# Optimization experiments

Measured on AMD Instinct MI355X. Metric: run time of the kernel, lower is better.

The kernel has to match this reference:

```python
import jax, jax.numpy as jnp
import numpy as np

B, L, H, E, D = 4, 2048, 8, 64, 64  # seq S == L (causal mask requires square scores)


def setup_inputs() -> dict:
    key = jax.random.key(0)
    k0, k1, k2, k3, k4 = jax.random.split(key, 5)
    queries = jax.random.normal(k0, (B, L, H, E), jnp.float32)
    keys = jax.random.normal(k1, (B, L, H, E), jnp.float32)
    values = jax.random.normal(k2, (B, L, H, D), jnp.float32)
    # per-sample learned de-stationary scale (positive) and bias
    tau = jax.random.uniform(k3, (B, 1, 1), jnp.float32, 0.5, 1.5)
    delta = jax.random.normal(k4, (B, 1, L), jnp.float32) * 0.1
    return {"queries": queries, "keys": keys, "values": values, "tau": tau, "delta": delta}


def reference(queries, keys, values, tau, delta):
    Bq, Lq, Hq, Eq = queries.shape
    S = keys.shape[1]
    scale = 1.0 / jnp.sqrt(jnp.asarray(Eq, jnp.float32))
    # torch path: rearrange('b s h d l -> (b d) s h l') with s=h=d=1 -> [B,1,1,1] / [B,1,1,S]
    tau_b = tau.reshape(Bq, 1, 1, 1)
    delta_b = delta.reshape(Bq, 1, 1, -1)[..., :S]
    # scores: [B, H, L, S]
    scores = jnp.einsum('blhe,bshe->bhls', queries, keys) * tau_b + delta_b
    causal = jnp.triu(jnp.ones((Lq, S), bool), k=1)  # True above diagonal -> masked
    scores = jnp.where(causal, -jnp.inf, scores)
    A = jax.nn.softmax(scale * scores, axis=-1)  # dropout is identity in eval/reference
    V = jnp.einsum('bhls,bshd->blhd', A, values)  # [B, L, H, D]
    return V
```

## Files before the change

kernel.cpp:

```cpp
#include <hip/hip_runtime.h>
#include <hip/hip_bf16.h>

#define Bsz 4
#define Lsz 2048
#define Hsz 8

typedef __attribute__((ext_vector_type(8))) short bf16x8;
typedef __attribute__((ext_vector_type(4))) short bf16x4;
typedef __attribute__((ext_vector_type(4))) float f32x4;

__device__ __forceinline__ short f2bs(float f) {
    union { float f; unsigned u; } v; v.f = f;
    unsigned r = v.u + 0x7FFFu + ((v.u >> 16) & 1u);
    return (short)(r >> 16);
}
__device__ __forceinline__ short f2bs_rh(float f) {
    return (short)((__float_as_uint(f) + 0x8000u) >> 16);
}

__device__ __forceinline__ void stage16(const short* g, short* l) {
    __builtin_amdgcn_global_load_lds(
        (const __attribute__((address_space(1))) unsigned int*)g,
        (__attribute__((address_space(3))) unsigned int*)l,
        16, 0, 0);
}

__global__ __launch_bounds__(256) void prep_kv(
    const float* __restrict__ ksrc, const float* __restrict__ vsrc,
    short* __restrict__ Kf, short* __restrict__ Vf)
{
    __shared__ float Tl[64][65];
    const int raw = blockIdx.x;
    const int tid = threadIdx.x;
    const bool isK = raw < Bsz*Hsz*32;
    const int bid = isK ? raw : raw - Bsz*Hsz*32;
    const int tl = bid & 31, bh = bid >> 5;
    const int b = bh >> 3, h = bh & 7;

    const int row = tid >> 2, c0 = (tid & 3) * 16;
    const float* src = (isK ? ksrc : vsrc)
                     + (((size_t)b*Lsz + tl*64 + row)*Hsz + h)*64 + c0;
    *(float4*)&Tl[row][c0]      = *(const float4*)(src);
    *(float4*)&Tl[row][c0 + 4]  = *(const float4*)(src + 4);
    *(float4*)&Tl[row][c0 + 8]  = *(const float4*)(src + 8);
    *(float4*)&Tl[row][c0 + 12] = *(const float4*)(src + 12);
    __syncthreads();

    const int lane = tid & 63, ln = lane & 15, quad = lane >> 4;
    if (isK) {
        short* dst = Kf + (size_t)bid * 4096;
        #pragma unroll
        for (int cc = 0; cc < 2; ++cc) {
            const int c  = (tid >> 6)*2 + cc;
            const int nt = c >> 1, eh = c & 1;
            const float* rp = &Tl[nt*16 + ln][eh*32 + quad*8];
            bf16x8 o = {f2bs(rp[0]),f2bs(rp[1]),f2bs(rp[2]),f2bs(rp[3]),
                        f2bs(rp[4]),f2bs(rp[5]),f2bs(rp[6]),f2bs(rp[7])};
            *(bf16x8*)(dst + c*512 + lane*8) = o;
        }
    } else {
        short* dst = Vf + (size_t)bid * 4096;
        #pragma unroll
        for (int cc = 0; cc < 2; ++cc) {
            const int cp  = (tid >> 6)*2 + cc;
            const int m16 = cp >> 1, nt0 = (cp & 1)*2;
            const int d   = m16*16 + ln;
            const int s0  = nt0*16 + quad*4;
            bf16x8 o = {f2bs(Tl[s0+0][d]),  f2bs(Tl[s0+1][d]),
                        f2bs(Tl[s0+2][d]),  f2bs(Tl[s0+3][d]),
                        f2bs(Tl[s0+16][d]), f2bs(Tl[s0+17][d]),
                        f2bs(Tl[s0+18][d]), f2bs(Tl[s0+19][d])};
            *(bf16x8*)(dst + cp*512 + lane*8) = o;
        }
    }
}

__global__ __launch_bounds__(256, 4) void dsattn_main(
    const float* __restrict__ q,
    const short* __restrict__ Kf,
    const short* __restrict__ Vf,
    const float* __restrict__ tau,
    const float* __restrict__ delta,
    float* __restrict__ out)
{
    __shared__ __align__(16) short Kb[2][4096];
    __shared__ __align__(16) short Vb[2][4096];
    __shared__ float dls[Lsz];

    const int tid  = threadIdx.x;
    const int wv   = tid >> 6;
    const int lane = tid & 63;
    const int ln   = lane & 15;
    const int quad = lane >> 4;

    const int bh = blockIdx.x;
    const int b  = bh >> 3, h = bh & 7;
    const int j  = blockIdx.y, aj = j & 7, gj = j >> 3;
    const int qt = (gj == 0) ? aj : (gj == 1) ? 15 - aj
                 : (gj == 2) ? 16 + aj : 31 - aj;
    const int q0 = qt * 64;
    const int T  = qt + 1;

    const float c2  = 0.125f * 1.44269504f;
    const float st2 = c2 * tau[b];

    const short* kt = Kf + (size_t)bh * (32*4096);
    const short* vt = Vf + (size_t)bh * (32*4096);

    {
        const float* dsrc = delta + (size_t)b*Lsz + tid*8;
        float4 a = *(const float4*)(dsrc);
        float4 c = *(const float4*)(dsrc + 4);
        a.x*=c2; a.y*=c2; a.z*=c2; a.w*=c2;
        c.x*=c2; c.y*=c2; c.z*=c2; c.w*=c2;
        *(float4*)&dls[tid*8]     = a;
        *(float4*)&dls[tid*8 + 4] = c;
    }

    #pragma unroll
    for (int u = 0; u < 4; ++u) {
        const int c = wv*4 + u;
        const short* g = ((c < 8) ? kt : vt) + (c & 7)*512 + lane*8;
        short* l = ((c < 8) ? &Kb[0][0] : &Vb[0][0]) + (c & 7)*512;
        stage16(g, l);
    }

    bf16x8 qf0, qf1;
    {
        const float* qrow = q + (((size_t)b*Lsz + q0 + wv*16 + ln)*Hsz + h)*64;
        float4 a0 = *(const float4*)(qrow + quad*8);
        float4 a1 = *(const float4*)(qrow + quad*8 + 4);
        float4 b0 = *(const float4*)(qrow + 32 + quad*8);
        float4 b1 = *(const float4*)(qrow + 32 + quad*8 + 4);
        qf0 = (bf16x8){f2bs(a0.x),f2bs(a0.y),f2bs(a0.z),f2bs(a0.w),
                       f2bs(a1.x),f2bs(a1.y),f2bs(a1.z),f2bs(a1.w)};
        qf1 = (bf16x8){f2bs(b0.x),f2bs(b0.y),f2bs(b0.z),f2bs(b0.w),
                       f2bs(b1.x),f2bs(b1.y),f2bs(b1.z),f2bs(b1.w)};
    }

    f32x4 oacc[4];
    #pragma unroll
    for (int m = 0; m < 4; ++m) oacc[m] = (f32x4){0.f,0.f,0.f,0.f};
    float l_acc = 0.f;

    __syncthreads();

    for (int t = 0; t < T; ++t) {
        const int cur = t & 1;
        if (t + 1 < T) {
            const int nb = cur ^ 1;
            #pragma unroll
            for (int u = 0; u < 4; ++u) {
                const int c = wv*4 + u;
                const short* g = ((c < 8) ? kt : vt)
                               + (size_t)(t+1)*4096 + (c & 7)*512 + lane*8;
                short* l = ((c < 8) ? &Kb[nb][0] : &Vb[nb][0]) + (c & 7)*512;
                stage16(g, l);
            }
        }

        const short* Kc = &Kb[cur][0];
        const short* Vc = &Vb[cur][0];
        const int k0 = t*64;

        f32x4 sacc[4];
        #pragma unroll
        for (int nt = 0; nt < 4; ++nt) {
            bf16x8 kf0 = *(const bf16x8*)(Kc + (nt*2+0)*512 + lane*8);
            bf16x8 kf1 = *(const bf16x8*)(Kc + (nt*2+1)*512 + lane*8);
            f32x4 z = (f32x4){0.f,0.f,0.f,0.f};
            z = __builtin_amdgcn_mfma_f32_16x16x32_bf16(kf0, qf0, z, 0,0,0);
            sacc[nt] = __builtin_amdgcn_mfma_f32_16x16x32_bf16(kf1, qf1, z, 0,0,0);
        }

        f32x4 dlv[4];
        #pragma unroll
        for (int nt = 0; nt < 4; ++nt)
            dlv[nt] = *(const f32x4*)&dls[k0 + nt*16 + quad*4];

        if (t == qt) {
            const int qrow = q0 + wv*16 + ln;
            #pragma unroll
            for (int nt = 0; nt < 4; ++nt)
                #pragma unroll
                for (int r = 0; r < 4; ++r)
                    if (k0 + nt*16 + quad*4 + r > qrow) sacc[nt][r] = -1e30f;
        }
        bf16x4 pT[4];
        #pragma unroll
        for (int nt = 0; nt < 4; ++nt) {
            float p0 = __builtin_amdgcn_exp2f(fmaf(sacc[nt][0], st2, dlv[nt][0]));
            float p1 = __builtin_amdgcn_exp2f(fmaf(sacc[nt][1], st2, dlv[nt][1]));
            float p2 = __builtin_amdgcn_exp2f(fmaf(sacc[nt][2], st2, dlv[nt][2]));
            float p3 = __builtin_amdgcn_exp2f(fmaf(sacc[nt][3], st2, dlv[nt][3]));
            l_acc += (p0 + p1) + (p2 + p3);
            pT[nt] = (bf16x4){f2bs_rh(p0), f2bs_rh(p1), f2bs_rh(p2), f2bs_rh(p3)};
        }

        #pragma unroll
        for (int ntp = 0; ntp < 2; ++ntp)
            #pragma unroll
            for (int m16 = 0; m16 < 4; ++m16) {
                bf16x8 vv = *(const bf16x8*)(Vc + (m16*2+ntp)*512 + lane*8);
                bf16x4 v0 = (bf16x4){vv[0], vv[1], vv[2], vv[3]};
                bf16x4 v1 = (bf16x4){vv[4], vv[5], vv[6], vv[7]};
                oacc[m16] = __builtin_amdgcn_mfma_f32_16x16x16bf16_1k(
                    v0, pT[2*ntp+0], oacc[m16], 0,0,0);
                oacc[m16] = __builtin_amdgcn_mfma_f32_16x16x16bf16_1k(
                    v1, pT[2*ntp+1], oacc[m16], 0,0,0);
            }

        __syncthreads();
    }

    float lsum = l_acc;
    lsum += __shfl_xor(lsum, 16, 64);
    lsum += __shfl_xor(lsum, 32, 64);
    const float inv = 1.0f / lsum;
    const int qrow = q0 + wv*16 + ln;
    float* orow = out + (((size_t)b*Lsz + qrow)*Hsz + h)*64;
    #pragma unroll
    for (int m16 = 0; m16 < 4; ++m16) {
        float4 o = {oacc[m16][0]*inv, oacc[m16][1]*inv,
                    oacc[m16][2]*inv, oacc[m16][3]*inv};
        *(float4*)(orow + m16*16 + quad*4) = o;
    }
}

extern "C" void kernel_launch(void* const* d_in, const int* in_sizes, int n_in,
                              void* d_out, int out_size, void* d_ws, size_t ws_size,
                              hipStream_t stream) {
    (void)in_sizes; (void)n_in; (void)out_size; (void)ws_size;
    const float* q     = (const float*)d_in[0];
    const float* k     = (const float*)d_in[1];
    const float* v     = (const float*)d_in[2];
    const float* tau   = (const float*)d_in[3];
    const float* delta = (const float*)d_in[4];
    float* out = (float*)d_out;

    short* Kf = (short*)d_ws;
    short* Vf = (short*)d_ws + (size_t)(4*1024*1024);

    prep_kv<<<dim3(Bsz*Hsz*32*2), dim3(256), 0, stream>>>(k, v, Kf, Vf);
    dsattn_main<<<dim3(Bsz*Hsz, 32), dim3(256), 0, stream>>>(q, Kf, Vf, tau, delta, out);
}
```

Before: 126.9 us.

## Software-pipeline QK of next tile with softmax and PV of previous tile

Restructures the attention loop so that the QK MFMA for tile t runs alongside the exp/softmax and PV MFMA for tile t-1. Score registers alternate between two sets, and V fragments are preloaded into registers before each barrier. Staging is also reorganised so each wave issues four contiguous 16-byte global-to-LDS loads per tile, with pointer increments instead of recomputed addresses, and s_setprio is raised around the compute section. This aims to hide exp latency and LDS read latency behind matrix work, at the cost of higher register pressure and more complex prologue and epilogue code for the causal diagonal tile.

```diff
diff --git a/kernel.cpp b/kernel.cpp
--- a/kernel.cpp
+++ b/kernel.cpp
@@ -107,6 +107,19 @@
     const short* kt = Kf + (size_t)bh * (32*4096);
     const short* vt = Vf + (size_t)bh * (32*4096);
 
+    const short* gsrc = ((wv < 2) ? kt : vt) + (wv & 1)*2048 + lane*8;
+
+#define STAGE(buf) do {                                                     \
+        short* lb_ = (wv < 2 ? &Kb[(buf)][0] : &Vb[(buf)][0]) + (wv&1)*2048;\
+        stage16(gsrc + 0*512, lb_ + 0*512);                                 \
+        stage16(gsrc + 1*512, lb_ + 1*512);                                 \
+        stage16(gsrc + 2*512, lb_ + 2*512);                                 \
+        stage16(gsrc + 3*512, lb_ + 3*512);                                 \
+        gsrc += 4096;                                                       \
+    } while (0)
+
+    STAGE(0);
+
     {
         const float* dsrc = delta + (size_t)b*Lsz + tid*8;
         float4 a = *(const float4*)(dsrc);
@@ -115,14 +128,6 @@
         c.x*=c2; c.y*=c2; c.z*=c2; c.w*=c2;
         *(float4*)&dls[tid*8]     = a;
         *(float4*)&dls[tid*8 + 4] = c;
-    }
-
-    #pragma unroll
-    for (int u = 0; u < 4; ++u) {
-        const int c = wv*4 + u;
-        const short* g = ((c < 8) ? kt : vt) + (c & 7)*512 + lane*8;
-        short* l = ((c < 8) ? &Kb[0][0] : &Vb[0][0]) + (c & 7)*512;
-        stage16(g, l);
     }
 
     bf16x8 qf0, qf1;
@@ -141,76 +146,102 @@
     f32x4 oacc[4];
     #pragma unroll
     for (int m = 0; m < 4; ++m) oacc[m] = (f32x4){0.f,0.f,0.f,0.f};
+    f32x4 sE[4], sO[4];
+    bf16x8 vv[8];
+    bf16x4 pT[4];
     float l_acc = 0.f;
 
+#define QK(tt, SW) do {                                                     \
+        const short* Kc_ = &Kb[(tt)&1][0];                                  \
+        _Pragma("unroll")                                                   \
+        for (int nt = 0; nt < 4; ++nt) {                                    \
+            bf16x8 kf0_ = *(const bf16x8*)(Kc_ + (nt*2+0)*512 + lane*8);    \
+            bf16x8 kf1_ = *(const bf16x8*)(Kc_ + (nt*2+1)*512 + lane*8);    \
+            f32x4 z_ = (f32x4){0.f,0.f,0.f,0.f};                            \
+            z_ = __builtin_amdgcn_mfma_f32_16x16x32_bf16(kf0_, qf0, z_, 0,0,0); \
+            (SW)[nt] = __builtin_amdgcn_mfma_f32_16x16x32_bf16(kf1_, qf1, z_, 0,0,0); \
+        }                                                                   \
+    } while (0)
+
+#define SM(tm, SR) do {                                                     \
+        const int k0_ = (tm)*64;                                            \
+        _Pragma("unroll")                                                   \
+        for (int nt = 0; nt < 4; ++nt) {                                    \
+            f32x4 dlv_ = *(const f32x4*)&dls[k0_ + nt*16 + quad*4];         \
+            float p0_ = __builtin_amdgcn_exp2f(fmaf((SR)[nt][0], st2, dlv_[0])); \
+            float p1_ = __builtin_amdgcn_exp2f(fmaf((SR)[nt][1], st2, dlv_[1])); \
+            float p2_ = __builtin_amdgcn_exp2f(fmaf((SR)[nt][2], st2, dlv_[2])); \
+            float p3_ = __builtin_amdgcn_exp2f(fmaf((SR)[nt][3], st2, dlv_[3])); \
+            l_acc += (p0_ + p1_) + (p2_ + p3_);                             \
+            pT[nt] = (bf16x4){f2bs_rh(p0_), f2bs_rh(p1_),                   \
+                              f2bs_rh(p2_), f2bs_rh(p3_)};                  \
+        }                                                                   \
+    } while (0)
+
+#define PV() do {                                                           \
+        _Pragma("unroll")                                                   \
+        for (int ntp = 0; ntp < 2; ++ntp)                                   \
+            _Pragma("unroll")                                               \
+            for (int m16 = 0; m16 < 4; ++m16) {                             \
+                bf16x8 v8_ = vv[m16*2 + ntp];                               \
+                bf16x4 v0_ = (bf16x4){v8_[0], v8_[1], v8_[2], v8_[3]};      \
+                bf16x4 v1_ = (bf16x4){v8_[4], v8_[5], v8_[6], v8_[7]};      \
+                oacc[m16] = __builtin_amdgcn_mfma_f32_16x16x16bf16_1k(      \
+                    v0_, pT[2*ntp+0], oacc[m16], 0,0,0);                    \
+                oacc[m16] = __builtin_amdgcn_mfma_f32_16x16x16bf16_1k(      \
+                    v1_, pT[2*ntp+1], oacc[m16], 0,0,0);                    \
+            }                                                               \
+    } while (0)
+
+#define VLOAD(tt) do {                                                      \
+        const short* Vc_ = &Vb[(tt)&1][0];                                  \
+        _Pragma("unroll")                                                   \
+        for (int c = 0; c < 8; ++c)                                         \
+            vv[c] = *(const bf16x8*)(Vc_ + c*512 + lane*8);                 \
+    } while (0)
+
+#define BODY(tt, SW, SR) do {                                               \
+        if ((tt) + 1 < T) STAGE(((tt)+1)&1);                                \
+        __builtin_amdgcn_s_setprio(1);                                      \
+        QK((tt), SW);                  \
+        SM((tt)-1, SR);                \
+        PV();                          \
+        __builtin_amdgcn_s_setprio(0);                                      \
+        VLOAD(tt);                     \
+        __syncthreads();                                                    \
+    } while (0)
+
     __syncthreads();
 
-    for (int t = 0; t < T; ++t) {
-        const int cur = t & 1;
-        if (t + 1 < T) {
-            const int nb = cur ^ 1;
+    if (T > 1) STAGE(1);
+    __builtin_amdgcn_s_setprio(1);
+    QK(0, sE);
+    __builtin_amdgcn_s_setprio(0);
+    VLOAD(0);
+    __syncthreads();
+
+    int t = 1;
+    for (; t + 1 < T; t += 2) {
+        BODY(t,     sO, sE);
+        BODY(t + 1, sE, sO);
+    }
+    if (t < T) BODY(t, sO, sE);
+
+    if ((T - 1) & 1) {
+        #pragma unroll
+        for (int nt = 0; nt < 4; ++nt) sE[nt] = sO[nt];
+    }
+
+    {
+        const int k0 = (T - 1) * 64;
+        const int qrow = q0 + wv*16 + ln;
+        #pragma unroll
+        for (int nt = 0; nt < 4; ++nt)
             #pragma unroll
-            for (int u = 0; u < 4; ++u) {
-                const int c = wv*4 + u;
-                const short* g = ((c < 8) ? kt : vt)
-                               + (size_t)(t+1)*4096 + (c & 7)*512 + lane*8;
-                short* l = ((c < 8) ? &Kb[nb][0] : &Vb[nb][0]) + (c & 7)*512;
-                stage16(g, l);
-            }
-        }
-
-        const short* Kc = &Kb[cur][0];
-        const short* Vc = &Vb[cur][0];
-        const int k0 = t*64;
-
-        f32x4 sacc[4];
-        #pragma unroll
-        for (int nt = 0; nt < 4; ++nt) {
-            bf16x8 kf0 = *(const bf16x8*)(Kc + (nt*2+0)*512 + lane*8);
-            bf16x8 kf1 = *(const bf16x8*)(Kc + (nt*2+1)*512 + lane*8);
-            f32x4 z = (f32x4){0.f,0.f,0.f,0.f};
-            z = __builtin_amdgcn_mfma_f32_16x16x32_bf16(kf0, qf0, z, 0,0,0);
-            sacc[nt] = __builtin_amdgcn_mfma_f32_16x16x32_bf16(kf1, qf1, z, 0,0,0);
-        }
-
-        f32x4 dlv[4];
-        #pragma unroll
-        for (int nt = 0; nt < 4; ++nt)
-            dlv[nt] = *(const f32x4*)&dls[k0 + nt*16 + quad*4];
-
-        if (t == qt) {
-            const int qrow = q0 + wv*16 + ln;
-            #pragma unroll
-            for (int nt = 0; nt < 4; ++nt)
-                #pragma unroll
-                for (int r = 0; r < 4; ++r)
-                    if (k0 + nt*16 + quad*4 + r > qrow) sacc[nt][r] = -1e30f;
-        }
-        bf16x4 pT[4];
-        #pragma unroll
-        for (int nt = 0; nt < 4; ++nt) {
-            float p0 = __builtin_amdgcn_exp2f(fmaf(sacc[nt][0], st2, dlv[nt][0]));
-            float p1 = __builtin_amdgcn_exp2f(fmaf(sacc[nt][1], st2, dlv[nt][1]));
-            float p2 = __builtin_amdgcn_exp2f(fmaf(sacc[nt][2], st2, dlv[nt][2]));
-            float p3 = __builtin_amdgcn_exp2f(fmaf(sacc[nt][3], st2, dlv[nt][3]));
-            l_acc += (p0 + p1) + (p2 + p3);
-            pT[nt] = (bf16x4){f2bs_rh(p0), f2bs_rh(p1), f2bs_rh(p2), f2bs_rh(p3)};
-        }
-
-        #pragma unroll
-        for (int ntp = 0; ntp < 2; ++ntp)
-            #pragma unroll
-            for (int m16 = 0; m16 < 4; ++m16) {
-                bf16x8 vv = *(const bf16x8*)(Vc + (m16*2+ntp)*512 + lane*8);
-                bf16x4 v0 = (bf16x4){vv[0], vv[1], vv[2], vv[3]};
-                bf16x4 v1 = (bf16x4){vv[4], vv[5], vv[6], vv[7]};
-                oacc[m16] = __builtin_amdgcn_mfma_f32_16x16x16bf16_1k(
-                    v0, pT[2*ntp+0], oacc[m16], 0,0,0);
-                oacc[m16] = __builtin_amdgcn_mfma_f32_16x16x16bf16_1k(
-                    v1, pT[2*ntp+1], oacc[m16], 0,0,0);
-            }
-
-        __syncthreads();
+            for (int r = 0; r < 4; ++r)
+                if (k0 + nt*16 + quad*4 + r > qrow) sE[nt][r] = -1e30f;
+        SM(T - 1, sE);
+        PV();
     }
 
     float lsum = l_acc;
@@ -225,6 +256,12 @@
                     oacc[m16][2]*inv, oacc[m16][3]*inv};
         *(float4*)(orow + m16*16 + quad*4) = o;
     }
+#undef STAGE
+#undef QK
+#undef SM
+#undef PV
+#undef VLOAD
+#undef BODY
 }
 
 extern "C" void kernel_launch(void* const* d_in, const int* in_sizes, int n_in,
```

New measurement: 125.6 us. About the same (-1.0%).

## Split key tiles across waves with shared Q and cross-wave output reduction

Applied to the files above, without the earlier changes.

The main kernel now gives each wave a 16-key slice of every 64-key tile, and all four waves compute against the full 64-row query block, which is stored once in LDS. This replaces the old scheme where each wave owned 16 query rows. Partial outputs and row sums are combined through LDS at the end, and the scaled delta is precomputed by extra blocks in the prep kernel. Each wave stages only its own K/V chunks, using explicit vmcnt waits instead of a per-tile block barrier, and MFMA sections run at raised priority. The costs are 64 accumulator registers per lane and an LDS reduction epilogue, and the query-tile order is rearranged for load balance.

```diff
diff --git a/kernel.cpp b/kernel.cpp
--- a/kernel.cpp
+++ b/kernel.cpp
@@ -5,9 +5,9 @@
 #define Lsz 2048
 #define Hsz 8
 
-typedef __attribute__((ext_vector_type(8))) short bf16x8;
-typedef __attribute__((ext_vector_type(4))) short bf16x4;
-typedef __attribute__((ext_vector_type(4))) float f32x4;
+typedef __attribute__((ext_vector_type(8)))  short bf16x8;
+typedef __attribute__((ext_vector_type(4)))  short bf16x4;
+typedef __attribute__((ext_vector_type(4)))  float f32x4;
 
 __device__ __forceinline__ short f2bs(float f) {
     union { float f; unsigned u; } v; v.f = f;
@@ -27,11 +27,23 @@
 
 __global__ __launch_bounds__(256) void prep_kv(
     const float* __restrict__ ksrc, const float* __restrict__ vsrc,
-    short* __restrict__ Kf, short* __restrict__ Vf)
+    const float* __restrict__ delta,
+    short* __restrict__ Kf, short* __restrict__ Vf, float* __restrict__ Df)
 {
-    __shared__ float Tl[64][65];
     const int raw = blockIdx.x;
     const int tid = threadIdx.x;
+    if (raw >= 2*Bsz*Hsz*32) {
+        const float c2 = 0.125f * 1.44269504f;
+        const int base = ((raw - 2*Bsz*Hsz*32)*256 + tid) * 16;
+        #pragma unroll
+        for (int u = 0; u < 4; ++u) {
+            float4 v = *(const float4*)(delta + base + u*4);
+            v.x*=c2; v.y*=c2; v.z*=c2; v.w*=c2;
+            *(float4*)(Df + base + u*4) = v;
+        }
+        return;
+    }
+    __shared__ float Tl[64][65];
     const bool isK = raw < Bsz*Hsz*32;
     const int bid = isK ? raw : raw - Bsz*Hsz*32;
     const int tl = bid & 31, bh = bid >> 5;
@@ -52,8 +64,8 @@
         #pragma unroll
         for (int cc = 0; cc < 2; ++cc) {
             const int c  = (tid >> 6)*2 + cc;
-            const int nt = c >> 1, eh = c & 1;
-            const float* rp = &Tl[nt*16 + ln][eh*32 + quad*8];
+            const int kq = c >> 1, eb = c & 1;
+            const float* rp = &Tl[kq*16 + ln][eb*32 + quad*8];
             bf16x8 o = {f2bs(rp[0]),f2bs(rp[1]),f2bs(rp[2]),f2bs(rp[3]),
                         f2bs(rp[4]),f2bs(rp[5]),f2bs(rp[6]),f2bs(rp[7])};
             *(bf16x8*)(dst + c*512 + lane*8) = o;
@@ -62,15 +74,16 @@
         short* dst = Vf + (size_t)bid * 4096;
         #pragma unroll
         for (int cc = 0; cc < 2; ++cc) {
-            const int cp  = (tid >> 6)*2 + cc;
-            const int m16 = cp >> 1, nt0 = (cp & 1)*2;
-            const int d   = m16*16 + ln;
-            const int s0  = nt0*16 + quad*4;
-            bf16x8 o = {f2bs(Tl[s0+0][d]),  f2bs(Tl[s0+1][d]),
-                        f2bs(Tl[s0+2][d]),  f2bs(Tl[s0+3][d]),
-                        f2bs(Tl[s0+16][d]), f2bs(Tl[s0+17][d]),
-                        f2bs(Tl[s0+18][d]), f2bs(Tl[s0+19][d])};
-            *(bf16x8*)(dst + cp*512 + lane*8) = o;
+            const int c   = (tid >> 6)*2 + cc;
+            const int kq  = c >> 1, dgp = c & 1;
+            const int s0  = kq*16 + quad*4;
+            const int d0  = dgp*32 + ln;
+            const int d1  = dgp*32 + 16 + ln;
+            bf16x8 o = {f2bs(Tl[s0+0][d0]), f2bs(Tl[s0+1][d0]),
+                        f2bs(Tl[s0+2][d0]), f2bs(Tl[s0+3][d0]),
+                        f2bs(Tl[s0+0][d1]), f2bs(Tl[s0+1][d1]),
+                        f2bs(Tl[s0+2][d1]), f2bs(Tl[s0+3][d1])};
+            *(bf16x8*)(dst + c*512 + lane*8) = o;
         }
     }
 }
@@ -79,152 +92,206 @@
     const float* __restrict__ q,
     const short* __restrict__ Kf,
     const short* __restrict__ Vf,
+    const float* __restrict__ Df,
     const float* __restrict__ tau,
-    const float* __restrict__ delta,
     float* __restrict__ out)
 {
     __shared__ __align__(16) short Kb[2][4096];
     __shared__ __align__(16) short Vb[2][4096];
-    __shared__ float dls[Lsz];
+    __shared__ __align__(16) short Qs[4096];
 
     const int tid  = threadIdx.x;
-    const int wv   = tid >> 6;
+    const int kq   = tid >> 6;
     const int lane = tid & 63;
     const int ln   = lane & 15;
     const int quad = lane >> 4;
 
     const int bh = blockIdx.x;
     const int b  = bh >> 3, h = bh & 7;
-    const int j  = blockIdx.y, aj = j & 7, gj = j >> 3;
-    const int qt = (gj == 0) ? aj : (gj == 1) ? 15 - aj
-                 : (gj == 2) ? 16 + aj : 31 - aj;
+    const int y = blockIdx.y, g8 = y >> 3, a = y & 7;
+    const int qt = (g8 == 0) ? 31 - 2*a : (g8 == 1) ? 2*a
+                 : (g8 == 2) ? 30 - 2*a : 2*a + 1;
     const int q0 = qt * 64;
     const int T  = qt + 1;
 
-    const float c2  = 0.125f * 1.44269504f;
-    const float st2 = c2 * tau[b];
-
-    const short* kt = Kf + (size_t)bh * (32*4096);
-    const short* vt = Vf + (size_t)bh * (32*4096);
+    const float st2 = (0.125f * 1.44269504f) * tau[b];
+
+    const short* gK = Kf + (size_t)bh*(32*4096) + kq*1024 + lane*8;
+    const short* gV = Vf + (size_t)bh*(32*4096) + kq*1024 + lane*8;
+    const float* Dfp = Df + (size_t)b*Lsz + kq*16 + quad*4;
+
+    short* const myK0 = &Kb[0][kq*1024];
+    short* const myV0 = &Vb[0][kq*1024];
+
+#define STAGE(buf) do {                                                     \
+        short* k_ = (buf) ? myK0 + 4096 : myK0;                             \
+        short* v_ = (buf) ? myV0 + 4096 : myV0;                             \
+        stage16(gK + 0*512, k_ + 0*512);                                    \
+        stage16(gK + 1*512, k_ + 1*512);                                    \
+        stage16(gV + 0*512, v_ + 0*512);                                    \
+        stage16(gV + 1*512, v_ + 1*512);                                    \
+        gK += 4096; gV += 4096;                                             \
+        __builtin_amdgcn_sched_barrier(0);                                  \
+    } while (0)
+#define WAITN(n) do {                                                       \
+        asm volatile("s_waitcnt vmcnt(" #n ")" ::: "memory");               \
+        __builtin_amdgcn_sched_barrier(0);                                  \
+    } while (0)
+
+    STAGE(0);
+    f32x4 dlv_c = *(const f32x4*)(Dfp); Dfp += 64;
 
     {
-        const float* dsrc = delta + (size_t)b*Lsz + tid*8;
-        float4 a = *(const float4*)(dsrc);
-        float4 c = *(const float4*)(dsrc + 4);
-        a.x*=c2; a.y*=c2; a.z*=c2; a.w*=c2;
-        c.x*=c2; c.y*=c2; c.z*=c2; c.w*=c2;
-        *(float4*)&dls[tid*8]     = a;
-        *(float4*)&dls[tid*8 + 4] = c;
-    }
-
-    #pragma unroll
-    for (int u = 0; u < 4; ++u) {
-        const int c = wv*4 + u;
-        const short* g = ((c < 8) ? kt : vt) + (c & 7)*512 + lane*8;
-        short* l = ((c < 8) ? &Kb[0][0] : &Vb[0][0]) + (c & 7)*512;
-        stage16(g, l);
-    }
-
-    bf16x8 qf0, qf1;
-    {
-        const float* qrow = q + (((size_t)b*Lsz + q0 + wv*16 + ln)*Hsz + h)*64;
+        const float* qrow = q + (((size_t)b*Lsz + q0 + kq*16 + ln)*Hsz + h)*64;
         float4 a0 = *(const float4*)(qrow + quad*8);
         float4 a1 = *(const float4*)(qrow + quad*8 + 4);
         float4 b0 = *(const float4*)(qrow + 32 + quad*8);
         float4 b1 = *(const float4*)(qrow + 32 + quad*8 + 4);
-        qf0 = (bf16x8){f2bs(a0.x),f2bs(a0.y),f2bs(a0.z),f2bs(a0.w),
-                       f2bs(a1.x),f2bs(a1.y),f2bs(a1.z),f2bs(a1.w)};
-        qf1 = (bf16x8){f2bs(b0.x),f2bs(b0.y),f2bs(b0.z),f2bs(b0.w),
-                       f2bs(b1.x),f2bs(b1.y),f2bs(b1.z),f2bs(b1.w)};
-    }
-
-    f32x4 oacc[4];
+        bf16x8 q0f = {f2bs(a0.x),f2bs(a0.y),f2bs(a0.z),f2bs(a0.w),
+                      f2bs(a1.x),f2bs(a1.y),f2bs(a1.z),f2bs(a1.w)};
+        bf16x8 q1f = {f2bs(b0.x),f2bs(b0.y),f2bs(b0.z),f2bs(b0.w),
+                      f2bs(b1.x),f2bs(b1.y),f2bs(b1.z),f2bs(b1.w)};
+        *(bf16x8*)(&Qs[(kq*2+0)*512 + lane*8]) = q0f;
+        *(bf16x8*)(&Qs[(kq*2+1)*512 + lane*8]) = q1f;
+    }
+
+    f32x4 oacc[4][4];
     #pragma unroll
-    for (int m = 0; m < 4; ++m) oacc[m] = (f32x4){0.f,0.f,0.f,0.f};
-    float l_acc = 0.f;
-
-    __syncthreads();
-
-    for (int t = 0; t < T; ++t) {
-        const int cur = t & 1;
-        if (t + 1 < T) {
-            const int nb = cur ^ 1;
+    for (int dg = 0; dg < 4; ++dg)
+        #pragma unroll
+        for (int qg = 0; qg < 4; ++qg)
+            oacc[dg][qg] = (f32x4){0.f,0.f,0.f,0.f};
+    float l_acc[4] = {0.f,0.f,0.f,0.f};
+
+    __syncthreads();
+
+#define TILE_BODY(t_, MASKED, HASNEXT) do {                                 \
+        const short* Kc_ = ((t_) & 1) ? myK0 + 4096 : myK0;                 \
+        const short* Vc_ = ((t_) & 1) ? myV0 + 4096 : myV0;                 \
+        f32x4 dlv_n_;                                                       \
+        if (HASNEXT) {                                                      \
+            STAGE(((t_)+1) & 1);                                            \
+            dlv_n_ = *(const f32x4*)(Dfp); Dfp += 64;                       \
+        }                                                                   \
+        if (HASNEXT) WAITN(8); else WAITN(3);            \
+        bf16x8 kf0_ = *(const bf16x8*)(Kc_ + 0*512 + lane*8);               \
+        bf16x8 kf1_ = *(const bf16x8*)(Kc_ + 1*512 + lane*8);               \
+        f32x4 sacc_[4];                                                     \
+        __builtin_amdgcn_s_setprio(1);                                      \
+        _Pragma("unroll")                                                   \
+        for (int qg = 0; qg < 4; ++qg) {                                    \
+            bf16x8 qa_ = *(const bf16x8*)(&Qs[(qg*2+0)*512 + lane*8]);      \
+            bf16x8 qb_ = *(const bf16x8*)(&Qs[(qg*2+1)*512 + lane*8]);      \
+            f32x4 z_ = (f32x4){0.f,0.f,0.f,0.f};                            \
+            z_ = __builtin_amdgcn_mfma_f32_16x16x32_bf16(kf0_, qa_, z_, 0,0,0); \
+            sacc_[qg] = __builtin_amdgcn_mfma_f32_16x16x32_bf16(kf1_, qb_, z_, 0,0,0); \
+        }                                                                   \
+        __builtin_amdgcn_s_setprio(0);                                      \
+        if (MASKED) {                                                       \
+            _Pragma("unroll")                                               \
+            for (int qg = 0; qg < 4; ++qg)                                  \
+                _Pragma("unroll")                                           \
+                for (int r = 0; r < 4; ++r)                                 \
+                    if (kq*16 + quad*4 + r > qg*16 + ln) sacc_[qg][r] = -1e30f; \
+        }                                                                   \
+        bf16x4 pT_[4];                                                      \
+        _Pragma("unroll")                                                   \
+        for (int qg = 0; qg < 4; ++qg) {                                    \
+            float p0_ = __builtin_amdgcn_exp2f(fmaf(sacc_[qg][0], st2, dlv_c[0])); \
+            float p1_ = __builtin_amdgcn_exp2f(fmaf(sacc_[qg][1], st2, dlv_c[1])); \
+            float p2_ = __builtin_amdgcn_exp2f(fmaf(sacc_[qg][2], st2, dlv_c[2])); \
+            float p3_ = __builtin_amdgcn_exp2f(fmaf(sacc_[qg][3], st2, dlv_c[3])); \
+            l_acc[qg] += (p0_ + p1_) + (p2_ + p3_);                         \
+            pT_[qg] = (bf16x4){f2bs_rh(p0_), f2bs_rh(p1_),                  \
+                               f2bs_rh(p2_), f2bs_rh(p3_)};                 \
+        }                                                                   \
+        if (HASNEXT) dlv_c = dlv_n_;                                        \
+        if (HASNEXT) WAITN(5); else WAITN(0);         \
+        bf16x4 vf_[4];                                                      \
+        _Pragma("unroll")                                                   \
+        for (int dg = 0; dg < 4; ++dg)                                      \
+            vf_[dg] = *(const bf16x4*)(Vc_ + (dg>>1)*512 + lane*8 + (dg&1)*4); \
+        __builtin_amdgcn_s_setprio(1);                                      \
+        _Pragma("unroll")                                                   \
+        for (int dg = 0; dg < 4; ++dg)                                      \
+            _Pragma("unroll")                                               \
+            for (int qg = 0; qg < 4; ++qg)                                  \
+                oacc[dg][qg] = __builtin_amdgcn_mfma_f32_16x16x16bf16_1k(   \
+                    vf_[dg], pT_[qg], oacc[dg][qg], 0,0,0);                 \
+        __builtin_amdgcn_s_setprio(0);                                      \
+    } while (0)
+
+    for (int t = 0; t < T - 1; ++t) TILE_BODY(t, false, true);
+    TILE_BODY(T - 1, true, false);
+
+    float lq[4];
+    #pragma unroll
+    for (int qg = 0; qg < 4; ++qg) {
+        float s = l_acc[qg];
+        s += __shfl_xor(s, 16, 64);
+        s += __shfl_xor(s, 32, 64);
+        lq[qg] = s;
+    }
+    float* KbF = (float*)&Kb[0][0];
+    float* VbF = (float*)&Vb[0][0];
+    float* lred = (float*)&Qs[0];
+    __syncthreads();
+
+    if (lane < 16)
+        #pragma unroll
+        for (int qg = 0; qg < 4; ++qg) lred[kq*64 + qg*16 + ln] = lq[qg];
+    if (kq == 1 || kq == 3) {
+        float* dst = (kq == 1) ? KbF : VbF;
+        #pragma unroll
+        for (int dg = 0; dg < 4; ++dg)
             #pragma unroll
-            for (int u = 0; u < 4; ++u) {
-                const int c = wv*4 + u;
-                const short* g = ((c < 8) ? kt : vt)
-                               + (size_t)(t+1)*4096 + (c & 7)*512 + lane*8;
-                short* l = ((c < 8) ? &Kb[nb][0] : &Vb[nb][0]) + (c & 7)*512;
-                stage16(g, l);
+            for (int qg = 0; qg < 4; ++qg)
+                *(f32x4*)(dst + (dg*4+qg)*256 + lane*4) = oacc[dg][qg];
+    }
+    __syncthreads();
+    if (kq == 0 || kq == 2) {
+        const float* srcp = (kq == 0) ? KbF : VbF;
+        #pragma unroll
+        for (int dg = 0; dg < 4; ++dg)
+            #pragma unroll
+            for (int qg = 0; qg < 4; ++qg) {
+                f32x4 v = *(const f32x4*)(srcp + (dg*4+qg)*256 + lane*4);
+                oacc[dg][qg][0] += v[0]; oacc[dg][qg][1] += v[1];
+                oacc[dg][qg][2] += v[2]; oacc[dg][qg][3] += v[3];
+            }
+    }
+    __syncthreads();
+    if (kq == 2) {
+        #pragma unroll
+        for (int dg = 0; dg < 4; ++dg)
+            #pragma unroll
+            for (int qg = 0; qg < 4; ++qg)
+                *(f32x4*)(KbF + (dg*4+qg)*256 + lane*4) = oacc[dg][qg];
+    }
+    __syncthreads();
+    if (kq == 0) {
+        float inv[4];
+        #pragma unroll
+        for (int qg = 0; qg < 4; ++qg)
+            inv[qg] = 1.0f / (lred[qg*16 + ln] + lred[64 + qg*16 + ln]
+                            + lred[128 + qg*16 + ln] + lred[192 + qg*16 + ln]);
+        #pragma unroll
+        for (int qg = 0; qg < 4; ++qg) {
+            float* orow = out + (((size_t)b*Lsz + q0 + qg*16 + ln)*Hsz + h)*64;
+            #pragma unroll
+            for (int dg = 0; dg < 4; ++dg) {
+                f32x4 v = *(const f32x4*)(KbF + (dg*4+qg)*256 + lane*4);
+                float4 o = {(oacc[dg][qg][0] + v[0]) * inv[qg],
+                            (oacc[dg][qg][1] + v[1]) * inv[qg],
+                            (oacc[dg][qg][2] + v[2]) * inv[qg],
+                            (oacc[dg][qg][3] + v[3]) * inv[qg]};
+                *(float4*)(orow + dg*16 + quad*4) = o;
             }
         }
-
-        const short* Kc = &Kb[cur][0];
-        const short* Vc = &Vb[cur][0];
-        const int k0 = t*64;
-
-        f32x4 sacc[4];
-        #pragma unroll
-        for (int nt = 0; nt < 4; ++nt) {
-            bf16x8 kf0 = *(const bf16x8*)(Kc + (nt*2+0)*512 + lane*8);
-            bf16x8 kf1 = *(const bf16x8*)(Kc + (nt*2+1)*512 + lane*8);
-            f32x4 z = (f32x4){0.f,0.f,0.f,0.f};
-            z = __builtin_amdgcn_mfma_f32_16x16x32_bf16(kf0, qf0, z, 0,0,0);
-            sacc[nt] = __builtin_amdgcn_mfma_f32_16x16x32_bf16(kf1, qf1, z, 0,0,0);
-        }
-
-        f32x4 dlv[4];
-        #pragma unroll
-        for (int nt = 0; nt < 4; ++nt)
-            dlv[nt] = *(const f32x4*)&dls[k0 + nt*16 + quad*4];
-
-        if (t == qt) {
-            const int qrow = q0 + wv*16 + ln;
-            #pragma unroll
-            for (int nt = 0; nt < 4; ++nt)
-                #pragma unroll
-                for (int r = 0; r < 4; ++r)
-                    if (k0 + nt*16 + quad*4 + r > qrow) sacc[nt][r] = -1e30f;
-        }
-        bf16x4 pT[4];
-        #pragma unroll
-        for (int nt = 0; nt < 4; ++nt) {
-            float p0 = __builtin_amdgcn_exp2f(fmaf(sacc[nt][0], st2, dlv[nt][0]));
-            float p1 = __builtin_amdgcn_exp2f(fmaf(sacc[nt][1], st2, dlv[nt][1]));
-            float p2 = __builtin_amdgcn_exp2f(fmaf(sacc[nt][2], st2, dlv[nt][2]));
-            float p3 = __builtin_amdgcn_exp2f(fmaf(sacc[nt][3], st2, dlv[nt][3]));
-            l_acc += (p0 + p1) + (p2 + p3);
-            pT[nt] = (bf16x4){f2bs_rh(p0), f2bs_rh(p1), f2bs_rh(p2), f2bs_rh(p3)};
-        }
-
-        #pragma unroll
-        for (int ntp = 0; ntp < 2; ++ntp)
-            #pragma unroll
-            for (int m16 = 0; m16 < 4; ++m16) {
-                bf16x8 vv = *(const bf16x8*)(Vc + (m16*2+ntp)*512 + lane*8);
-                bf16x4 v0 = (bf16x4){vv[0], vv[1], vv[2], vv[3]};
-                bf16x4 v1 = (bf16x4){vv[4], vv[5], vv[6], vv[7]};
-                oacc[m16] = __builtin_amdgcn_mfma_f32_16x16x16bf16_1k(
-                    v0, pT[2*ntp+0], oacc[m16], 0,0,0);
-                oacc[m16] = __builtin_amdgcn_mfma_f32_16x16x16bf16_1k(
-                    v1, pT[2*ntp+1], oacc[m16], 0,0,0);
-            }
-
-        __syncthreads();
-    }
-
-    float lsum = l_acc;
-    lsum += __shfl_xor(lsum, 16, 64);
-    lsum += __shfl_xor(lsum, 32, 64);
-    const float inv = 1.0f / lsum;
-    const int qrow = q0 + wv*16 + ln;
-    float* orow = out + (((size_t)b*Lsz + qrow)*Hsz + h)*64;
-    #pragma unroll
-    for (int m16 = 0; m16 < 4; ++m16) {
-        float4 o = {oacc[m16][0]*inv, oacc[m16][1]*inv,
-                    oacc[m16][2]*inv, oacc[m16][3]*inv};
-        *(float4*)(orow + m16*16 + quad*4) = o;
-    }
+    }
+#undef STAGE
+#undef WAITN
+#undef TILE_BODY
 }
 
 extern "C" void kernel_launch(void* const* d_in, const int* in_sizes, int n_in,
@@ -240,7 +307,8 @@
 
     short* Kf = (short*)d_ws;
     short* Vf = (short*)d_ws + (size_t)(4*1024*1024);
-
-    prep_kv<<<dim3(Bsz*Hsz*32*2), dim3(256), 0, stream>>>(k, v, Kf, Vf);
-    dsattn_main<<<dim3(Bsz*Hsz, 32), dim3(256), 0, stream>>>(q, Kf, Vf, tau, delta, out);
-}
+    float* Df = (float*)((char*)d_ws + (size_t)(16*1024*1024));
+
+    prep_kv<<<dim3(Bsz*Hsz*32*2 + 2), dim3(256), 0, stream>>>(k, v, delta, Kf, Vf, Df);
+    dsattn_main<<<dim3(Bsz*Hsz, 32), dim3(256), 0, stream>>>(q, Kf, Vf, Df, tau, out);
+}
```

New measurement: 129.6 us. 2.1% more time.
